# Kernel tuning notes

Measured on AMD Instinct MI355X. Metric: run time of the kernel, lower is better.

The kernel has to match this reference:

```python
import jax, jax.numpy as jnp
import numpy as np

N = 8192
E = 262144
DIN = 512
DOUT = 256


def setup_inputs() -> dict:
    key = jax.random.key(0)
    k1, k2, k3, k4 = jax.random.split(key, 4)
    x = jax.random.normal(k1, (N, DIN), dtype=jnp.float32)
    edge_index = jax.random.randint(k2, (2, E), 0, N, dtype=jnp.int64)
    edge_weight = jax.random.uniform(k3, (E,), dtype=jnp.float32)
    W = jax.random.normal(k4, (DOUT, DIN), dtype=jnp.float32) * (1.0 / np.sqrt(DIN))
    return {"x": x, "edge_index": edge_index, "edge_weight": edge_weight, "W": W}


def reference(x, edge_index, edge_weight, W):
    n = x.shape[0]
    # Linear(dim_in, dim_out, bias=False): h = x @ W.T  -> [N, DOUT]
    h = x @ W.T
    # Dense adjacency: A[src, dst] += w (to_dense_adj sums duplicate edges)
    src, dst = edge_index[0], edge_index[1]
    A = jnp.zeros((n, n), dtype=x.dtype).at[src, dst].add(edge_weight)
    # degree from A BEFORE self-loops, then +1 from the added eye on degree_matrix
    deg = jnp.sum(A, axis=1) + 1.0
    # sqrt(inverse(diag(deg))) == diag(1/sqrt(deg)); apply as row scaling
    dinv_sqrt = 1.0 / jnp.sqrt(deg)  # [N]
    A = A + jnp.eye(n, dtype=x.dtype)  # self-loops on adjacency
    # x = D^{-1/2} @ (A.T @ (D^{-1/2} @ h))
    h = dinv_sqrt[:, None] * h
    h = A.T @ h
    h = dinv_sqrt[:, None] * h
    return h
```

## Files before the change

kernel.cpp:

```cpp
#include <hip/hip_runtime.h>

static constexpr int DIN = 512;
static constexpr int DOUT = 256;
static constexpr int CAP = 128;

typedef __attribute__((ext_vector_type(8))) short short8;
typedef __attribute__((ext_vector_type(4))) float f32x4;

__device__ inline unsigned short f2bf(float f) {
  unsigned int b = __float_as_uint(f);
  unsigned int r = (b + 0x7fffu + ((b >> 16) & 1u)) >> 16;
  return (unsigned short)r;
}
__device__ inline float bf_lo(unsigned int packed) { return __uint_as_float(packed << 16); }
__device__ inline float bf_hi(unsigned int packed) { return __uint_as_float(packed & 0xffff0000u); }

__device__ inline short8 cvt8(const float4 a, const float4 b) {
  short8 o;
  o[0] = (short)f2bf(a.x); o[1] = (short)f2bf(a.y);
  o[2] = (short)f2bf(a.z); o[3] = (short)f2bf(a.w);
  o[4] = (short)f2bf(b.x); o[5] = (short)f2bf(b.y);
  o[6] = (short)f2bf(b.z); o[7] = (short)f2bf(b.w);
  return o;
}

__global__ __launch_bounds__(256) void k_edges(
    const int* __restrict__ ei, const float* __restrict__ ew,
    const float* __restrict__ W,
    float* __restrict__ deg, int* __restrict__ cursor,
    uint2* __restrict__ bucket, unsigned short* __restrict__ wbb,
    int E, int EB) {
  const int b = blockIdx.x;
  if (b < EB) {
    int e = b * 256 + threadIdx.x;
    if (e < E) {
      int srcv = ei[e];
      int dstv = ei[E + e];
      float w = ew[e];
      atomicAdd(&deg[srcv], w);
      int pos = atomicAdd(&cursor[dstv], 1);
      if (pos < CAP) {
        uint2 v;
        v.x = (unsigned)srcv;
        v.y = __float_as_uint(w);
        bucket[(size_t)dstv * CAP + pos] = v;
      }
    }
  } else {
    long i = (long)(b - EB) * 256 + threadIdx.x;
    const float4* src = (const float4*)(W + i * 8);
    float4 a = src[0], bb = src[1];
    *(short8*)(wbb + i * 8) = cvt8(a, bb);
  }
}

__global__ __launch_bounds__(256) void k_gemm_mfma(
    const float* __restrict__ x, const unsigned short* __restrict__ wbb,
    const float* __restrict__ deg, unsigned short* __restrict__ h1b) {
  const int lane = threadIdx.x & 63;
  const int wv = threadIdx.x >> 6;
  const int bm = blockIdx.x * 16;
  const int colb = wv * 64;
  const int r = lane & 15;
  const int kg = lane >> 4;
  f32x4 acc[4] = {};
  const float* arow = x + (size_t)(bm + r) * DIN + kg * 8;
  const unsigned short* brow0 = wbb + (size_t)(colb + r) * DIN + kg * 8;
#pragma unroll
  for (int k0 = 0; k0 < DIN; k0 += 32) {
    float4 a0 = *(const float4*)(arow + k0);
    float4 a1 = *(const float4*)(arow + k0 + 4);
    short8 av = cvt8(a0, a1);
#pragma unroll
    for (int nt = 0; nt < 4; ++nt) {
      short8 bv = *(const short8*)(brow0 + (size_t)nt * 16 * DIN + k0);
      acc[nt] = __builtin_amdgcn_mfma_f32_16x16x32_bf16(av, bv, acc[nt], 0, 0, 0);
    }
  }
#pragma unroll
  for (int i = 0; i < 4; ++i) {
    int row = bm + kg * 4 + i;
    float sr = __frsqrt_rn(1.0f + deg[row]);
#pragma unroll
    for (int nt = 0; nt < 4; ++nt) {
      h1b[(size_t)row * DOUT + colb + nt * 16 + r] = f2bf(sr * acc[nt][i]);
    }
  }
}

__global__ __launch_bounds__(256, 4) void k_gather(
    const unsigned short* __restrict__ h1b, const float* __restrict__ deg,
    const int* __restrict__ cursor, const uint2* __restrict__ bucket,
    float* __restrict__ out) {
  const int lane = threadIdx.x & 63;
  const int wv = threadIdx.x >> 6;
  const int dst = blockIdx.x * 4 + wv;
  const int cl = lane & 31;
  const int half = lane >> 5;
  const int cnt = min(cursor[dst], CAP);

  const uint4 selfv = *(const uint4*)(h1b + (size_t)dst * DOUT + cl * 8);
  const float sd = __frsqrt_rn(1.0f + deg[dst]);

  float acc[8] = {};

  for (int base = 0; base < cnt; base += 64) {
    const int c = min(64, cnt - base);
    int sv = 0;
    float wl = 0.f;
    if (lane < c) {
      uint2 ev = bucket[(size_t)dst * CAP + base + lane];
      sv = (int)ev.x;
      wl = __uint_as_float(ev.y);
    }
    const int npair = ((c + 15) >> 4) << 3;
    for (int j = 0; j < npair; j += 8) {
      uint4 rbuf[8];
#pragma unroll
      for (int u = 0; u < 8; ++u) {
        int src = __shfl(sv, 2 * (j + u) + half);
        rbuf[u] = *(const uint4*)(h1b + (size_t)src * DOUT + cl * 8);
      }
#pragma unroll
      for (int u = 0; u < 8; ++u) {
        float w = __shfl(wl, 2 * (j + u) + half);
        acc[0] = fmaf(w, bf_lo(rbuf[u].x), acc[0]);
        acc[1] = fmaf(w, bf_hi(rbuf[u].x), acc[1]);
        acc[2] = fmaf(w, bf_lo(rbuf[u].y), acc[2]);
        acc[3] = fmaf(w, bf_hi(rbuf[u].y), acc[3]);
        acc[4] = fmaf(w, bf_lo(rbuf[u].z), acc[4]);
        acc[5] = fmaf(w, bf_hi(rbuf[u].z), acc[5]);
        acc[6] = fmaf(w, bf_lo(rbuf[u].w), acc[6]);
        acc[7] = fmaf(w, bf_hi(rbuf[u].w), acc[7]);
      }
    }
  }

#pragma unroll
  for (int k = 0; k < 8; ++k) acc[k] += __shfl_xor(acc[k], 32);

  if (half == 0) {
    float4 o0v, o1v;
    o0v.x = sd * (bf_lo(selfv.x) + acc[0]);
    o0v.y = sd * (bf_hi(selfv.x) + acc[1]);
    o0v.z = sd * (bf_lo(selfv.y) + acc[2]);
    o0v.w = sd * (bf_hi(selfv.y) + acc[3]);
    o1v.x = sd * (bf_lo(selfv.z) + acc[4]);
    o1v.y = sd * (bf_hi(selfv.z) + acc[5]);
    o1v.z = sd * (bf_lo(selfv.w) + acc[6]);
    o1v.w = sd * (bf_hi(selfv.w) + acc[7]);
    float* op = out + (size_t)dst * DOUT + cl * 8;
    *(float4*)op = o0v;
    *(float4*)(op + 4) = o1v;
  }
}

extern "C" void kernel_launch(void* const* d_in, const int* in_sizes, int n_in,
                              void* d_out, int out_size, void* d_ws, size_t ws_size,
                              hipStream_t stream) {
  const float* x = (const float*)d_in[0];
  const int* ei = (const int*)d_in[1];
  const float* ew = (const float*)d_in[2];
  const float* W = (const float*)d_in[3];
  float* out = (float*)d_out;

  const int n = in_sizes[0] / DIN;
  const int E = in_sizes[2];

  char* p = (char*)d_ws;
  auto alloc = [&](size_t bytes) {
    char* q = p;
    p += (bytes + 255) & ~(size_t)255;
    return q;
  };
  unsigned short* h1b = (unsigned short*)alloc((size_t)n * DOUT * 2);
  unsigned short* wbb = (unsigned short*)alloc((size_t)DOUT * DIN * 2);
  float* deg   = (float*)alloc((size_t)n * 4 * 2);
  int* cursor  = (int*)(deg + n);
  uint2* bucket = (uint2*)alloc((size_t)n * CAP * 8);

  const int EB = (E + 255) / 256;
  const int WB = (DOUT * DIN / 8 + 255) / 256;

  hipMemsetAsync(deg, 0, (size_t)n * 8, stream);
  k_edges<<<EB + WB, 256, 0, stream>>>(ei, ew, W, deg, cursor, bucket, wbb, E, EB);
  k_gemm_mfma<<<n / 16, 256, 0, stream>>>(x, wbb, deg, h1b);
  k_gather<<<n / 4, 256, 0, stream>>>(h1b, deg, cursor, bucket, out);
}
```

Measured before the change: 74.05 us.

## Split gather into two column-half passes with four edges per wave step

Splits the sparse gather into two launches, each covering 128 of the 256 output columns. Within a wave, 16 lanes now cover one edge's half-row and 4 edges are processed at once, with a two-step shuffle reduction at the end. The intent is to halve the h1b working set per pass so gathered rows stay in L2/MALL and random-access reads hit cache more often. In exchange the bucket and cursor are read twice, there is an extra launch, and each global load fetches only 256 bytes of contiguous data per edge.

```diff
diff --git a/kernel.cpp b/kernel.cpp
--- a/kernel.cpp
+++ b/kernel.cpp
@@ -88,58 +88,67 @@
   }
 }
 
-__global__ __launch_bounds__(256, 4) void k_gather(
+__device__ inline void gather_chunk_half(float acc[8], int sv, float wl, int c,
+                                         const unsigned short* hbase, int cl,
+                                         int eslot) {
+  const int nb = (c + 3) >> 2;
+  for (int j0 = 0; j0 < nb; j0 += 8) {
+    uint4 rbuf[8];
+#pragma unroll
+    for (int u = 0; u < 8; ++u) {
+      int idx = (j0 + u) * 4 + eslot;
+      int src = __shfl(sv, idx);
+      rbuf[u] = *(const uint4*)(hbase + (size_t)src * DOUT + cl * 8);
+    }
+#pragma unroll
+    for (int u = 0; u < 8; ++u) {
+      float w = __shfl(wl, (j0 + u) * 4 + eslot);
+      acc[0] = fmaf(w, bf_lo(rbuf[u].x), acc[0]);
+      acc[1] = fmaf(w, bf_hi(rbuf[u].x), acc[1]);
+      acc[2] = fmaf(w, bf_lo(rbuf[u].y), acc[2]);
+      acc[3] = fmaf(w, bf_hi(rbuf[u].y), acc[3]);
+      acc[4] = fmaf(w, bf_lo(rbuf[u].z), acc[4]);
+      acc[5] = fmaf(w, bf_hi(rbuf[u].z), acc[5]);
+      acc[6] = fmaf(w, bf_lo(rbuf[u].w), acc[6]);
+      acc[7] = fmaf(w, bf_hi(rbuf[u].w), acc[7]);
+    }
+  }
+}
+
+__global__ __launch_bounds__(256, 4) void k_gather_half(
     const unsigned short* __restrict__ h1b, const float* __restrict__ deg,
     const int* __restrict__ cursor, const uint2* __restrict__ bucket,
-    float* __restrict__ out) {
+    float* __restrict__ out, int colofs) {
   const int lane = threadIdx.x & 63;
   const int wv = threadIdx.x >> 6;
-  const int dst = blockIdx.x * 4 + wv;
-  const int cl = lane & 31;
-  const int half = lane >> 5;
-  const int cnt = min(cursor[dst], CAP);
+  const int d = blockIdx.x * 4 + wv;
+  const int cl = lane & 15;
+  const int eslot = lane >> 4;
+  const int cnt = min(cursor[d], CAP);
+  const unsigned short* hbase = h1b + colofs;
 
-  const uint4 selfv = *(const uint4*)(h1b + (size_t)dst * DOUT + cl * 8);
-  const float sd = __frsqrt_rn(1.0f + deg[dst]);
+  const uint4 selfv = *(const uint4*)(hbase + (size_t)d * DOUT + cl * 8);
+  const float sd = __frsqrt_rn(1.0f + deg[d]);
+
+  uint2 ev0; ev0.x = 0u; ev0.y = 0u;
+  uint2 ev1; ev1.x = 0u; ev1.y = 0u;
+  if (lane < cnt) ev0 = bucket[(size_t)d * CAP + lane];
+  if (64 + lane < cnt) ev1 = bucket[(size_t)d * CAP + 64 + lane];
 
   float acc[8] = {};
+  gather_chunk_half(acc, (int)ev0.x, __uint_as_float(ev0.y), min(cnt, 64),
+                    hbase, cl, eslot);
+  if (cnt > 64)
+    gather_chunk_half(acc, (int)ev1.x, __uint_as_float(ev1.y), cnt - 64,
+                      hbase, cl, eslot);
 
-  for (int base = 0; base < cnt; base += 64) {
-    const int c = min(64, cnt - base);
-    int sv = 0;
-    float wl = 0.f;
-    if (lane < c) {
-      uint2 ev = bucket[(size_t)dst * CAP + base + lane];
-      sv = (int)ev.x;
-      wl = __uint_as_float(ev.y);
-    }
-    const int npair = ((c + 15) >> 4) << 3;
-    for (int j = 0; j < npair; j += 8) {
-      uint4 rbuf[8];
 #pragma unroll
-      for (int u = 0; u < 8; ++u) {
-        int src = __shfl(sv, 2 * (j + u) + half);
-        rbuf[u] = *(const uint4*)(h1b + (size_t)src * DOUT + cl * 8);
-      }
-#pragma unroll
-      for (int u = 0; u < 8; ++u) {
-        float w = __shfl(wl, 2 * (j + u) + half);
-        acc[0] = fmaf(w, bf_lo(rbuf[u].x), acc[0]);
-        acc[1] = fmaf(w, bf_hi(rbuf[u].x), acc[1]);
-        acc[2] = fmaf(w, bf_lo(rbuf[u].y), acc[2]);
-        acc[3] = fmaf(w, bf_hi(rbuf[u].y), acc[3]);
-        acc[4] = fmaf(w, bf_lo(rbuf[u].z), acc[4]);
-        acc[5] = fmaf(w, bf_hi(rbuf[u].z), acc[5]);
-        acc[6] = fmaf(w, bf_lo(rbuf[u].w), acc[6]);
-        acc[7] = fmaf(w, bf_hi(rbuf[u].w), acc[7]);
-      }
-    }
+  for (int k = 0; k < 8; ++k) {
+    acc[k] += __shfl_xor(acc[k], 16);
+    acc[k] += __shfl_xor(acc[k], 32);
   }
 
-#pragma unroll
-  for (int k = 0; k < 8; ++k) acc[k] += __shfl_xor(acc[k], 32);
-
-  if (half == 0) {
+  if (eslot == 0) {
     float4 o0v, o1v;
     o0v.x = sd * (bf_lo(selfv.x) + acc[0]);
     o0v.y = sd * (bf_hi(selfv.x) + acc[1]);
@@ -149,7 +158,7 @@
     o1v.y = sd * (bf_hi(selfv.z) + acc[5]);
     o1v.z = sd * (bf_lo(selfv.w) + acc[6]);
     o1v.w = sd * (bf_hi(selfv.w) + acc[7]);
-    float* op = out + (size_t)dst * DOUT + cl * 8;
+    float* op = out + (size_t)d * DOUT + colofs + cl * 8;
     *(float4*)op = o0v;
     *(float4*)(op + 4) = o1v;
   }
@@ -185,5 +194,6 @@
   hipMemsetAsync(deg, 0, (size_t)n * 8, stream);
   k_edges<<<EB + WB, 256, 0, stream>>>(ei, ew, W, deg, cursor, bucket, wbb, E, EB);
   k_gemm_mfma<<<n / 16, 256, 0, stream>>>(x, wbb, deg, h1b);
-  k_gather<<<n / 4, 256, 0, stream>>>(h1b, deg, cursor, bucket, out);
+  k_gather_half<<<n / 4, 256, 0, stream>>>(h1b, deg, cursor, bucket, out, 0);
+  k_gather_half<<<n / 4, 256, 0, stream>>>(h1b, deg, cursor, bucket, out, 128);
 }
```

Measured after the change: 78.84 us. +6.5%, slower.
